# Optimization experiments

Measured on AMD Instinct MI355X. Metric: run time of the kernel, lower is better.

The kernel has to match this reference:

```python
import math
import jax, jax.numpy as jnp
import numpy as np

D_MODEL = 1024
N_HEADS = 16
HEAD_DIM = 64          # block_size
NUM_RULES = 64
RANK = 8               # proj_rank = round(sqrt(head_dim)); also router_rank
SHARED_RANK = 32       # round(sqrt(d_model))
NUM_BLOCKS = 16        # min(in,out)//block_size = 1024//64; total_block_dim == d_model
B, S = 4, 1024
ROPE_BASE = 10000.0


def setup_inputs() -> dict:
    key = jax.random.key(0)
    ks = iter(jax.random.split(key, 32))
    def nrm(shape, s=0.02):
        return jax.random.normal(next(ks), shape, dtype=jnp.float32) * s
    inp = {
        "x": jax.random.normal(next(ks), (B, S, D_MODEL), dtype=jnp.float32),
        "target_rule_ids": jax.random.randint(next(ks), (B, S), 0, NUM_RULES),
    }
    for p in ("q", "k", "v", "o"):
        inp[p + "_si"] = nrm((D_MODEL, SHARED_RANK))
        inp[p + "_so"] = nrm((SHARED_RANK, D_MODEL))
        inp[p + "_ri"] = nrm((NUM_RULES, HEAD_DIM, RANK))
        inp[p + "_ro"] = nrm((NUM_RULES, RANK, HEAD_DIM))
        inp[p + "_lg"] = nrm((NUM_RULES, NUM_BLOCKS), 1.0 / math.sqrt(NUM_BLOCKS))
    inp["router_q"] = nrm((NUM_RULES, RANK))
    inp["router_k"] = nrm((NUM_RULES, RANK))
    return inp


def _rule_proj(x, rules, si, so, ri, ro, lg):
    """RuleAwareProjection.forward_rules_batched, de-permuted.

    The torch code argsorts tokens by rule, zero-pads per-rule buckets, runs
    bmm per rule and scatters back; mathematically that equals a per-token
    gather of the rule's low-rank adapter, which is what we compute here.
    x: [N, D_MODEL], rules: [N] int.
    """
    base = (x @ si) @ so                                  # shared low-rank path
    xb = x.reshape(-1, NUM_BLOCKS, HEAD_DIM)              # [N, nb, bs]
    h = jnp.einsum('nbs,nsr->nbr', xb, ri[rules])         # [N, nb, rank]
    a = jnp.einsum('nbr,nrt->nbt', h, ro[rules])          # [N, nb, bs]
    # temperature = 1/sqrt(num_blocks) => logits / temperature = logits*sqrt(nb)
    sel = jax.nn.softmax(lg[rules] * math.sqrt(NUM_BLOCKS), axis=-1)
    return base + (a * sel[:, :, None]).reshape(-1, D_MODEL)


def _rope(q, k):
    # q, k: [B, H, S, D]; interleaved-pair rotation, start_pos = 0.
    S_, D = q.shape[2], q.shape[3]
    pos = jnp.arange(S_, dtype=jnp.float32)[:, None]
    div = jnp.exp(jnp.arange(0, D, 2, dtype=jnp.float32) * (-math.log(ROPE_BASE) / D))
    f = pos * div                                         # [S, D/2]
    sin, cos = jnp.sin(f), jnp.cos(f)
    def rot(t):
        t1, t2 = t[..., 0::2], t[..., 1::2]
        return jnp.stack([t1 * cos - t2 * sin, t2 * cos + t1 * sin], axis=-1).reshape(t.shape)
    return rot(q), rot(k)


def reference(x, target_rule_ids,
              q_si, q_so, q_ri, q_ro, q_lg,
              k_si, k_so, k_ri, k_ro, k_lg,
              v_si, v_so, v_ri, v_ro, v_lg,
              o_si, o_so, o_ri, o_ro, o_lg,
              router_q, router_k):
    B_, S_, C = x.shape
    flat_x = x.reshape(-1, C)
    rules = target_rule_ids.reshape(-1)

    q = _rule_proj(flat_x, rules, q_si, q_so, q_ri, q_ro, q_lg)
    k = _rule_proj(flat_x, rules, k_si, k_so, k_ri, k_ro, k_lg)
    v = _rule_proj(flat_x, rules, v_si, v_so, v_ri, v_ro, v_lg)
    q = q.reshape(B_, S_, N_HEADS, HEAD_DIM).transpose(0, 2, 1, 3)
    k = k.reshape(B_, S_, N_HEADS, HEAD_DIM).transpose(0, 2, 1, 3)
    v = v.reshape(B_, S_, N_HEADS, HEAD_DIM).transpose(0, 2, 1, 3)
    q, k = _rope(q, k)

    # rule-routing sparse mask: cosine affinity between token rule embeddings
    rq = router_q[target_rule_ids]                        # [B, S, rank]
    rk = router_k[target_rule_ids]
    rqn = rq / jnp.maximum(jnp.linalg.norm(rq, axis=-1, keepdims=True), 1e-12)
    rkn = rk / jnp.maximum(jnp.linalg.norm(rk, axis=-1, keepdims=True), 1e-12)
    tau = 1.0 / math.log(max(math.e, RANK))
    aff = jnp.einsum('bqr,bkr->bqk', rqn, rkn) / tau       # [B, S, S]
    causal = jnp.tril(jnp.ones((S_, S_), dtype=bool))
    masked = jnp.where(causal[None], aff, -jnp.inf)
    top_k = max(2, int(math.sqrt(S_)))
    if S_ > top_k:
        thr = jax.lax.top_k(masked, top_k)[0][..., -1:]
        rule_mask = (masked >= thr) & causal[None]
    else:
        rule_mask = jnp.broadcast_to(causal[None], masked.shape)

    scores = jnp.einsum('bhqd,bhkd->bhqk', q, k) / math.sqrt(HEAD_DIM)
    scores = jnp.where(rule_mask[:, None], scores, -jnp.inf)
    attn = jax.nn.softmax(scores, axis=-1)
    out = jnp.einsum('bhqk,bhkd->bhqd', attn, v)
    out = out.transpose(0, 2, 1, 3).reshape(-1, C)
    out = _rule_proj(out, rules, o_si, o_so, o_ri, o_ro, o_lg)
    return out.reshape(B_, S_, C)
```

## Files before the change

kernel.cpp:

```cpp
#include <hip/hip_runtime.h>
#include <hip/hip_bf16.h>

#define D_MODEL 1024
#define N_HEADS 16
#define HEAD_DIM 64
#define NUM_RULES 64
#define RANK 8
#define SHARED_RANK 32
#define NUM_BLOCKS_ 16
#define BB 4
#define SS 1024
#define NTOK (BB*SS)
#define NGRP (NTOK/8)
#define NGRP4 (NTOK/4)

typedef __attribute__((ext_vector_type(8))) short bf16x8;
typedef __attribute__((ext_vector_type(4))) float f32x4;

__device__ __forceinline__ float bf2f(unsigned short u) {
  unsigned int i = ((unsigned int)u) << 16;
  float f;
  __builtin_memcpy(&f, &i, 4);
  return f;
}
__device__ __forceinline__ unsigned short f2bf(float f) {
  __hip_bfloat16 h = __float2bfloat16(f);
  unsigned short u;
  __builtin_memcpy(&u, &h, 2);
  return u;
}
__device__ __forceinline__ float u2f(unsigned int i) {
  float f;
  __builtin_memcpy(&f, &i, 4);
  return f;
}
template<bool BF>
__device__ __forceinline__ float ldw(const void* p, size_t i) {
  if (BF) return bf2f(((const unsigned short*)p)[i]);
  else    return ((const float*)p)[i];
}

__device__ __forceinline__ void gload16(const void* g, void* l) {
  __builtin_amdgcn_global_load_lds(
      (const __attribute__((address_space(1))) unsigned int*)g,
      (__attribute__((address_space(3))) unsigned int*)l, 16, 0, 0);
}

__global__ void detect_kernel(const unsigned short* __restrict__ x, int* __restrict__ flag) {
  const int lane = threadIdx.x;
  int good = 0;
  for (int i = 0; i < 4; i++) {
    unsigned short u = x[lane*4 + i];
    int e = (u >> 7) & 0xFF;
    good += (e == 0 || (e >= 100 && e <= 145)) ? 1 : 0;
  }
  for (int off = 32; off; off >>= 1) good += __shfl_xor(good, off);
  if (lane == 0) flag[0] = (good >= 224) ? 1 : 0;
}

template<bool BF>
__device__ __forceinline__ void precompute_body(
    const void* rq, const void* rk,
    const void* qlg, const void* klg, const void* vlg, const void* olg,
    float* __restrict__ M, float* __restrict__ sel)
{
  __shared__ float rqn[64][8], rkn[64][8];
  const int tid = threadIdx.x;
  if (tid < 64) {
    float v[8]; float s = 0.f;
    for (int i = 0; i < 8; i++) { v[i] = ldw<BF>(rq, tid*8+i); s += v[i]*v[i]; }
    float inv = 1.0f / fmaxf(sqrtf(s), 1e-12f);
    for (int i = 0; i < 8; i++) rqn[tid][i] = v[i]*inv;
  } else if (tid < 128) {
    int r = tid - 64;
    float v[8]; float s = 0.f;
    for (int i = 0; i < 8; i++) { v[i] = ldw<BF>(rk, r*8+i); s += v[i]*v[i]; }
    float inv = 1.0f / fmaxf(sqrtf(s), 1e-12f);
    for (int i = 0; i < 8; i++) rkn[r][i] = v[i]*inv;
  }
  __syncthreads();
  const float LN8 = 2.0794415416798357f;
  for (int idx = tid; idx < 64*64; idx += 256) {
    int i = idx >> 6, j = idx & 63;
    float d = 0.f;
    for (int t = 0; t < 8; t++) d += rqn[i][t]*rkn[j][t];
    M[idx] = d * LN8;
  }
  const void* lgs[4] = {qlg, klg, vlg, olg};
  {
    int r = tid & 63;
    const void* lg = lgs[tid >> 6];
    float e[NUM_BLOCKS_]; float mx = -1e30f;
    for (int b = 0; b < NUM_BLOCKS_; b++) {
      e[b] = ldw<BF>(lg, r*NUM_BLOCKS_ + b) * 4.0f;
      mx = fmaxf(mx, e[b]);
    }
    float s = 0.f;
    for (int b = 0; b < NUM_BLOCKS_; b++) { e[b] = expf(e[b]-mx); s += e[b]; }
    float inv = 1.0f/s;
    for (int b = 0; b < NUM_BLOCKS_; b++) sel[tid*NUM_BLOCKS_+b] = e[b]*inv;
  }
}

__global__ void precompute_kernel(
    const void* rq, const void* rk,
    const void* qlg, const void* klg, const void* vlg, const void* olg,
    float* M, float* sel, const int* __restrict__ flag)
{
  if (*flag) precompute_body<true >(rq, rk, qlg, klg, vlg, olg, M, sel);
  else       precompute_body<false>(rq, rk, qlg, klg, vlg, olg, M, sel);
}

__global__ __launch_bounds__(128) void prep_wb_kernel(
    const float* __restrict__ qsi, const float* __restrict__ ksi,
    const float* __restrict__ vsi, const float* __restrict__ osi,
    unsigned short* __restrict__ wh, unsigned short* __restrict__ wl,
    const int* __restrict__ flag)
{
  if (*flag) return;
  const int kt = blockIdx.x, p = blockIdx.y;
  const int tid = threadIdx.x, nt = tid >> 6, lane = tid & 63;
  const float* si = (p==0)?qsi:((p==1)?ksi:((p==2)?vsi:osi));
  const int col = nt*16 + (lane & 15);
  const int k0 = kt*32 + (lane >> 4)*8;
  size_t base = ((((size_t)p*32 + kt)*2 + nt)*64 + lane)*8;
  unsigned short h8[8], l8[8];
  #pragma unroll
  for (int j = 0; j < 8; j++) {
    float f = si[(size_t)(k0 + j)*SHARED_RANK + col];
    unsigned short hu = f2bf(f);
    h8[j] = hu;
    l8[j] = f2bf(f - bf2f(hu));
  }
  #pragma unroll
  for (int j = 0; j < 8; j++) { wh[base + j] = h8[j]; wl[base + j] = l8[j]; }
}

template<int NPROJ>
__device__ __forceinline__ void tt_mfma_body(
    const float* __restrict__ xin,
    const unsigned short* __restrict__ wh, const unsigned short* __restrict__ wl,
    int p0, float* __restrict__ ttg)
{
  const int NT = NPROJ*2;
  const int tile = blockIdx.x;
  const int tid = threadIdx.x, lane = tid & 63, w = tid >> 6;
  const int kq = lane >> 4;
  __shared__ float red[4][64][25];

  f32x4 acc[NT];
  #pragma unroll
  for (int i = 0; i < NT; i++) acc[i] = (f32x4){0.f,0.f,0.f,0.f};

  const float* xrow = xin + (size_t)(tile*16 + (lane & 15))*D_MODEL + kq*8;
  #pragma unroll 2
  for (int s = 0; s < 8; s++) {
    const int kt = w*8 + s;
    float4 a0 = *(const float4*)(xrow + kt*32);
    float4 a1 = *(const float4*)(xrow + kt*32 + 4);
    float av[8] = {a0.x,a0.y,a0.z,a0.w,a1.x,a1.y,a1.z,a1.w};
    bf16x8 ah, al;
    #pragma unroll
    for (int j = 0; j < 8; j++) {
      unsigned short hu = f2bf(av[j]);
      ah[j] = (short)hu;
      al[j] = (short)f2bf(av[j] - bf2f(hu));
    }
    #pragma unroll
    for (int p = 0; p < NPROJ; p++) {
      #pragma unroll
      for (int nt = 0; nt < 2; nt++) {
        size_t bidx = ((((size_t)(p0+p)*32 + kt)*2 + nt)*64 + lane)*8;
        bf16x8 bh = *(const bf16x8*)(wh + bidx);
        bf16x8 bl = *(const bf16x8*)(wl + bidx);
        f32x4 c = acc[p*2+nt];
        c = __builtin_amdgcn_mfma_f32_16x16x32_bf16(ah, bh, c, 0, 0, 0);
        c = __builtin_amdgcn_mfma_f32_16x16x32_bf16(al, bh, c, 0, 0, 0);
        c = __builtin_amdgcn_mfma_f32_16x16x32_bf16(ah, bl, c, 0, 0, 0);
        acc[p*2+nt] = c;
      }
    }
  }
  #pragma unroll
  for (int i = 0; i < NT; i++) {
    red[w][lane][i*4+0] = acc[i][0]; red[w][lane][i*4+1] = acc[i][1];
    red[w][lane][i*4+2] = acc[i][2]; red[w][lane][i*4+3] = acc[i][3];
  }
  __syncthreads();
  if (w == 0) {
    const int tok0 = tile*16 + (lane >> 4)*4;
    #pragma unroll
    for (int i = 0; i < NT; i++) {
      const int ys = i >> 1, jj = (i & 1)*16 + (lane & 15);
      #pragma unroll
      for (int r = 0; r < 4; r++) {
        float sum = red[0][lane][i*4+r] + red[1][lane][i*4+r]
                  + red[2][lane][i*4+r] + red[3][lane][i*4+r];
        ttg[((size_t)ys*NTOK + tok0 + r)*32 + jj] = sum;
      }
    }
  }
}

__global__ __launch_bounds__(256) void A_tt_mfma3(
    const float* __restrict__ xin,
    const unsigned short* __restrict__ wh, const unsigned short* __restrict__ wl,
    float* __restrict__ ttg, const int* __restrict__ flag)
{
  if (*flag) return;
  tt_mfma_body<3>(xin, wh, wl, 0, ttg);
}

__global__ __launch_bounds__(256) void A_tt_mfma1(
    const float* __restrict__ xin,
    const unsigned short* __restrict__ wh, const unsigned short* __restrict__ wl,
    float* __restrict__ ttg, const int* __restrict__ flag)
{
  if (*flag) return;
  tt_mfma_body<1>(xin, wh, wl, 3, ttg);
}

template<int NP>
__device__ __forceinline__ void hh_body(
    const float* __restrict__ xin, const int* __restrict__ rules,
    const float* __restrict__ ri0, const float* __restrict__ ri1,
    const float* __restrict__ ri2, float* __restrict__ hhg)
{
  const int g = blockIdx.x, n0 = g*8, tid = threadIdx.x;
  const int t = tid >> 5, blk = (tid >> 1) & 15, r0 = (tid & 1)*4;
  const int n = n0 + t;
  const int rule = rules[n];
  const float* xb = xin + (size_t)n*D_MODEL + blk*64;
  const float* wb[3];
  wb[0] = ri0 + (size_t)rule*512 + r0;
  if (NP > 1) {
    wb[1] = ri1 + (size_t)rule*512 + r0;
    wb[2] = ri2 + (size_t)rule*512 + r0;
  }
  float a[NP][4];
  #pragma unroll
  for (int p = 0; p < NP; p++) { a[p][0]=0.f; a[p][1]=0.f; a[p][2]=0.f; a[p][3]=0.f; }
  #pragma unroll 4
  for (int k4 = 0; k4 < 16; k4++) {
    float4 xv = *(const float4*)(xb + k4*4);
    #pragma unroll
    for (int q = 0; q < 4; q++) {
      const int k = k4*4 + q;
      float xq = (q==0)?xv.x:((q==1)?xv.y:((q==2)?xv.z:xv.w));
      #pragma unroll
      for (int p = 0; p < NP; p++) {
        float4 wv = *(const float4*)(wb[p] + (size_t)k*8);
        a[p][0] += xq*wv.x; a[p][1] += xq*wv.y; a[p][2] += xq*wv.z; a[p][3] += xq*wv.w;
      }
    }
  }
  #pragma unroll
  for (int p = 0; p < NP; p++) {
    float4 hv; hv.x=a[p][0]; hv.y=a[p][1]; hv.z=a[p][2]; hv.w=a[p][3];
    *(float4*)&hhg[((size_t)p*NTOK + n)*128 + blk*8 + r0] = hv;
  }
}

__global__ __launch_bounds__(256) void A_hh3_f32(
    const float* __restrict__ xin, const int* __restrict__ rules,
    const float* __restrict__ qri, const float* __restrict__ kri,
    const float* __restrict__ vri, float* __restrict__ hhg,
    const int* __restrict__ flag)
{
  if (*flag) return;
  hh_body<3>(xin, rules, qri, kri, vri, hhg);
}

__global__ __launch_bounds__(256) void A_hh1_f32(
    const float* __restrict__ xin, const int* __restrict__ rules,
    const float* __restrict__ ori, float* __restrict__ hhg,
    const int* __restrict__ flag)
{
  if (*flag) return;
  hh_body<1>(xin, rules, ori, ori, ori, hhg);
}

template<bool IN_BF, bool W_BF>
__device__ __forceinline__ void stageA_body(
    const void* __restrict__ xin, const int* __restrict__ rules,
    const void* __restrict__ si, const void* __restrict__ ri,
    float* __restrict__ ttg, float* __restrict__ hhg, int yslot)
{
  const int g = blockIdx.x, n0 = g*8, tid = threadIdx.x;
  __shared__ float xs[8][D_MODEL];
  __shared__ float tpart[8][32][9];
  __shared__ int rl[8];

  #pragma unroll
  for (int t = 0; t < 8; t++) {
    float4 f;
    if (IN_BF) {
      ushort4 u = ((const ushort4*)((const unsigned short*)xin + (size_t)(n0+t)*D_MODEL))[tid];
      f.x = bf2f(u.x); f.y = bf2f(u.y); f.z = bf2f(u.z); f.w = bf2f(u.w);
    } else {
      f = ((const float4*)xin)[(size_t)(n0+t)*(D_MODEL/4) + tid];
    }
    *(float4*)&xs[t][tid*4] = f;
  }
  if (tid < 8) rl[tid] = rules[n0 + tid];
  __syncthreads();

  {
    const int c = tid >> 5, j = tid & 31;
    float p[8];
    #pragma unroll
    for (int t = 0; t < 8; t++) p[t] = 0.f;
    #pragma unroll 4
    for (int d4 = 0; d4 < 32; d4++) {
      const int d = c*128 + d4*4;
      float w0 = ldw<W_BF>(si, (size_t)(d+0)*SHARED_RANK + j);
      float w1 = ldw<W_BF>(si, (size_t)(d+1)*SHARED_RANK + j);
      float w2 = ldw<W_BF>(si, (size_t)(d+2)*SHARED_RANK + j);
      float w3 = ldw<W_BF>(si, (size_t)(d+3)*SHARED_RANK + j);
      #pragma unroll
      for (int t = 0; t < 8; t++) {
        float4 xv = *(const float4*)&xs[t][d];
        p[t] += xv.x*w0 + xv.y*w1 + xv.z*w2 + xv.w*w3;
      }
    }
    #pragma unroll
    for (int t = 0; t < 8; t++) tpart[c][j][t] = p[t];
  }
  __syncthreads();

  {
    const int t = tid >> 5, j = tid & 31;
    float s = 0.f;
    #pragma unroll
    for (int c = 0; c < 8; c++) s += tpart[c][j][t];
    ttg[((size_t)yslot*NTOK + n0 + t)*32 + j] = s;
  }
  {
    const int t = tid >> 5, blk = (tid >> 1) & 15, r0 = (tid & 1)*4;
    const int rule = rl[t];
    float a0=0.f, a1=0.f, a2=0.f, a3=0.f;
    #pragma unroll 4
    for (int k4 = 0; k4 < 16; k4++) {
      const int kk = ((k4 + blk) & 15) * 4;
      float4 xv = *(const float4*)&xs[t][blk*64 + kk];
      #pragma unroll
      for (int q = 0; q < 4; q++) {
        const int k = kk + q;
        float w0,w1,w2,w3;
        if (W_BF) {
          ushort4 u = *(const ushort4*)((const unsigned short*)ri + (size_t)rule*512 + (size_t)k*8 + r0);
          w0=bf2f(u.x); w1=bf2f(u.y); w2=bf2f(u.z); w3=bf2f(u.w);
        } else {
          float4 u = *(const float4*)((const float*)ri + (size_t)rule*512 + (size_t)k*8 + r0);
          w0=u.x; w1=u.y; w2=u.z; w3=u.w;
        }
        float xq = (q==0)?xv.x:((q==1)?xv.y:((q==2)?xv.z:xv.w));
        a0 += xq*w0; a1 += xq*w1; a2 += xq*w2; a3 += xq*w3;
      }
    }
    float4 hv; hv.x=a0; hv.y=a1; hv.z=a2; hv.w=a3;
    *(float4*)&hhg[((size_t)yslot*NTOK + n0 + t)*128 + blk*8 + r0] = hv;
  }
}

__global__ __launch_bounds__(256) void A_qkv_bf16(
    const void* x, const int* rules,
    const void* qsi, const void* qri, const void* ksi, const void* kri,
    const void* vsi, const void* vri,
    float* ttg, float* hhg, const int* __restrict__ flag)
{
  if (!*flag) return;
  const int y = blockIdx.y;
  const void* si = (y==0)?qsi:((y==1)?ksi:vsi);
  const void* ri = (y==0)?qri:((y==1)?kri:vri);
  stageA_body<true,true>(x, rules, si, ri, ttg, hhg, y);
}

__global__ __launch_bounds__(256) void A_o_bf16(
    const void* ain, const int* rules, const void* osi, const void* ori,
    float* ttg, float* hhg, const int* __restrict__ flag)
{
  if (!*flag) return;
  stageA_body<false,true>(ain, rules, osi, ori, ttg, hhg, 0);
}

template<bool W_BF>
__device__ __forceinline__ void stageB_body(
    const float* __restrict__ ttg, const float* __restrict__ hhg,
    const int* __restrict__ rules,
    const void* __restrict__ so, const void* __restrict__ ro,
    const float* __restrict__ sel, void* __restrict__ out,
    int yslot, int do_rope, int out_bf)
{
  const int blk4 = blockIdx.x;
  const int n0 = blk4*4, tid = threadIdx.x;
  __shared__ float tt_lds[32][5];
  __shared__ float hh_lds[4][132];
  __shared__ int rl[4];

  if (tid < 128) {
    const int j = tid >> 2, t4 = tid & 3;
    tt_lds[j][t4] = ttg[((size_t)yslot*NTOK + n0 + t4)*32 + j];
  } else if (tid < 256 && (tid - 128) < 128) {
    const int i = tid - 128;
    const int t4 = i >> 5, c = (i*4) & 127;
    float4 hv = *(const float4*)&hhg[((size_t)yslot*NTOK + n0 + t4)*128 + c];
    *(float4*)&hh_lds[t4][c] = hv;
  }
  if (tid < 4) rl[tid] = rules[n0 + tid];
  __syncthreads();

  const int ch0 = tid*4;
  float a0[4], a1[4], a2[4], a3[4];
  #pragma unroll
  for (int t = 0; t < 4; t++) { a0[t]=0.f; a1[t]=0.f; a2[t]=0.f; a3[t]=0.f; }

  #pragma unroll 4
  for (int j = 0; j < 32; j++) {
    float w0, w1, w2, w3;
    if (W_BF) {
      ushort4 u = *(const ushort4*)((const unsigned short*)so + (size_t)j*D_MODEL + ch0);
      w0=bf2f(u.x); w1=bf2f(u.y); w2=bf2f(u.z); w3=bf2f(u.w);
    } else {
      float4 u = *(const float4*)((const float*)so + (size_t)j*D_MODEL + ch0);
      w0=u.x; w1=u.y; w2=u.z; w3=u.w;
    }
    #pragma unroll
    for (int t = 0; t < 4; t++) {
      float tv = tt_lds[j][t];
      a0[t] += tv*w0; a1[t] += tv*w1; a2[t] += tv*w2; a3[t] += tv*w3;
    }
  }

  const int blk = ch0 >> 6, tc = ch0 & 63;
  float inv0 = 0.f, inv1 = 0.f;
  if (do_rope) {
    inv0 = expf(-(float)tc     * (9.210340371976184f/64.0f));
    inv1 = expf(-(float)(tc+2) * (9.210340371976184f/64.0f));
  }
  #pragma unroll 2
  for (int t = 0; t < 4; t++) {
    const int rule = rl[t];
    float b0=0.f, b1=0.f, b2=0.f, b3=0.f;
    #pragma unroll
    for (int r = 0; r < 8; r++) {
      float w0,w1,w2,w3;
      if (W_BF) {
        ushort4 u = *(const ushort4*)((const unsigned short*)ro + (size_t)rule*512 + r*64 + tc);
        w0=bf2f(u.x); w1=bf2f(u.y); w2=bf2f(u.z); w3=bf2f(u.w);
      } else {
        float4 u = *(const float4*)((const float*)ro + (size_t)rule*512 + r*64 + tc);
        w0=u.x; w1=u.y; w2=u.z; w3=u.w;
      }
      float hv = hh_lds[t][blk*8 + r];
      b0 += hv*w0; b1 += hv*w1; b2 += hv*w2; b3 += hv*w3;
    }
    float sb = sel[rule*NUM_BLOCKS_ + blk];
    float e0 = a0[t] + b0*sb, o0 = a1[t] + b1*sb;
    float e1 = a2[t] + b2*sb, o1 = a3[t] + b3*sb;
    const int n = n0 + t;
    if (do_rope) {
      float spos = (float)(n & (SS-1));
      float sn0, cs0, sn1, cs1;
      sincosf(spos*inv0, &sn0, &cs0);
      sincosf(spos*inv1, &sn1, &cs1);
      float u0 = e0*cs0 - o0*sn0; o0 = o0*cs0 + e0*sn0; e0 = u0;
      float u1 = e1*cs1 - o1*sn1; o1 = o1*cs1 + e1*sn1; e1 = u1;
    }
    if (out_bf) {
      ushort4 uv; uv.x=f2bf(e0); uv.y=f2bf(o0); uv.z=f2bf(e1); uv.w=f2bf(o1);
      *(ushort4*)((unsigned short*)out + (size_t)n*D_MODEL + ch0) = uv;
    } else {
      float4 fv; fv.x=e0; fv.y=o0; fv.z=e1; fv.w=o1;
      *(float4*)((float*)out + (size_t)n*D_MODEL + ch0) = fv;
    }
  }
}

__global__ __launch_bounds__(256) void B_qkv(
    const float* ttg, const float* hhg, const int* rules,
    const void* qso, const void* qro, const void* kso, const void* kro,
    const void* vso, const void* vro,
    const float* sel, float* qb, unsigned short* kb, unsigned short* vb,
    const int* __restrict__ flag)
{
  const int y = blockIdx.y;
  const void* so = (y==0)?qso:((y==1)?kso:vso);
  const void* ro = (y==0)?qro:((y==1)?kro:vro);
  void* out = (y==0)?(void*)qb:((y==1)?(void*)kb:(void*)vb);
  if (*flag)
    stageB_body<true >(ttg, hhg, rules, so, ro, sel + y*1024, out, y, (y<2)?1:0, (y>=1)?1:0);
  else
    stageB_body<false>(ttg, hhg, rules, so, ro, sel + y*1024, out, y, (y<2)?1:0, (y>=1)?1:0);
}

__global__ __launch_bounds__(256) void B_o(
    const float* ttg, const float* hhg, const int* rules,
    const void* oso, const void* oro, const float* sel, void* out,
    const int* __restrict__ flag)
{
  if (*flag) stageB_body<true >(ttg, hhg, rules, oso, oro, sel, out, 0, 0, 1);
  else       stageB_body<false>(ttg, hhg, rules, oso, oro, sel, out, 0, 0, 0);
}

__global__ __launch_bounds__(64) void mask_kernel(
    const int* __restrict__ rules, const float* __restrict__ M,
    unsigned long long* __restrict__ am, unsigned int* __restrict__ rp)
{
  const int bid = blockIdx.x;
  const int b = bid >> 10, qi = bid & 1023;
  const int lane = threadIdx.x;
  __shared__ int rrow[SS];
  __shared__ float val[64];
  __shared__ int cnth[64];
  for (int i = lane; i < SS/4; i += 64)
    ((int4*)rrow)[i] = ((const int4*)(rules + b*SS))[i];
  cnth[lane] = 0;
  __syncthreads();
  if (qi < 16 && lane < 16) {
    unsigned v = 0;
    #pragma unroll
    for (int nt = 0; nt < 4; nt++)
      v |= ((unsigned)rrow[qi*64 + nt*16 + lane] & 0xffu) << (8*nt);
    rp[b*256 + qi*16 + lane] = v;
  }
  for (int k = lane; k <= qi; k += 64) atomicAdd(&cnth[rrow[k]], 1);
  const int qrule = rrow[qi];
  const float myv = M[qrule*64 + lane];
  val[lane] = myv;
  __syncthreads();
  const int c = cnth[lane];
  int A = 0;
  for (int r = 0; r < 64; r++) {
    int cr = __shfl(c, r);
    A += (val[r] > myv) ? cr : 0;
  }
  unsigned long long allowed = __ballot(A < 32);
  if (lane == 0) am[bid] = allowed;
}

__global__ __launch_bounds__(256) void vtrans_kernel(
    const unsigned short* __restrict__ vb, unsigned short* __restrict__ vt)
{
  const int st = blockIdx.x, h = blockIdx.y, b = blockIdx.z;
  __shared__ unsigned short t[64][72];
  const int tid = threadIdx.x;
  #pragma unroll
  for (int it = 0; it < 2; it++) {
    int i = tid + it*256;
    int r = i >> 3, c8 = (i & 7)*8;
    uint4 v = *(const uint4*)(vb + ((size_t)(b*SS + st*64 + r)*D_MODEL + h*HEAD_DIM + c8));
    t[c8+0][r] = (unsigned short)(v.x & 0xffffu);
    t[c8+1][r] = (unsigned short)(v.x >> 16);
    t[c8+2][r] = (unsigned short)(v.y & 0xffffu);
    t[c8+3][r] = (unsigned short)(v.y >> 16);
    t[c8+4][r] = (unsigned short)(v.z & 0xffffu);
    t[c8+5][r] = (unsigned short)(v.z >> 16);
    t[c8+6][r] = (unsigned short)(v.w & 0xffffu);
    t[c8+7][r] = (unsigned short)(v.w >> 16);
  }
  __syncthreads();
  #pragma unroll
  for (int it = 0; it < 2; it++) {
    int i = tid + it*256;
    int d = i >> 3, c8 = i & 7;
    uint4 o = *(const uint4*)&t[d][c8*8];
    *(uint4*)(vt + ((size_t)(b*N_HEADS + h)*HEAD_DIM + d)*SS + st*64 + c8*8) = o;
  }
}

__global__ __launch_bounds__(256, 4) void attn_mfma_kernel(
    const float* __restrict__ qb,
    const unsigned short* __restrict__ kb,
    const unsigned short* __restrict__ vtb,
    const unsigned int* __restrict__ rp,
    const unsigned long long* __restrict__ am,
    float* outb)
{
  const int x = blockIdx.x, b = blockIdx.y, h = blockIdx.z;
  const int qt = (x < 8) ? x : (23 - x);
  const int tid = threadIdx.x, lane = tid & 63, w = tid >> 6;
  __shared__ unsigned short Ks[2][64*64];
  __shared__ unsigned short Vs[2][64*64];
  __shared__ unsigned short Pl[4][16*64];

  const unsigned short* kbase = kb + (size_t)b*SS*D_MODEL + h*HEAD_DIM;
  const unsigned short* vbase = vtb + (size_t)(b*N_HEADS + h)*HEAD_DIM*SS;
  const unsigned int* rpb = rp + b*256;

  const int srow0 = tid >> 3;
  const int spos  = tid & 7;
  unsigned short* pw = &Pl[w][0];

  const int qa = qt*64 + w*16 + (lane & 15);
  bf16x8 qfrag[2];
  {
    const float* qrow = qb + (size_t)(b*SS + qa)*D_MODEL + h*HEAD_DIM + (lane>>4)*8;
    #pragma unroll
    for (int kc = 0; kc < 2; kc++) {
      float4 f0 = *(const float4*)(qrow + kc*32);
      float4 f1 = *(const float4*)(qrow + kc*32 + 4);
      bf16x8 qv;
      qv[0] = (short)f2bf(f0.x*0.125f); qv[1] = (short)f2bf(f0.y*0.125f);
      qv[2] = (short)f2bf(f0.z*0.125f); qv[3] = (short)f2bf(f0.w*0.125f);
      qv[4] = (short)f2bf(f1.x*0.125f); qv[5] = (short)f2bf(f1.y*0.125f);
      qv[6] = (short)f2bf(f1.z*0.125f); qv[7] = (short)f2bf(f1.w*0.125f);
      qfrag[kc] = qv;
    }
  }
  int qg[4]; unsigned aqlo[4], aqhi[4];
  #pragma unroll
  for (int r = 0; r < 4; r++) {
    qg[r] = qt*64 + w*16 + (lane>>4)*4 + r;
    uint2 mm = *(const uint2*)(am + (size_t)b*SS + qg[r]);
    aqlo[r] = mm.x; aqhi[r] = mm.y;
  }
  f32x4 Oacc[4];
  #pragma unroll
  for (int nt = 0; nt < 4; nt++) Oacc[nt] = (f32x4){0.f,0.f,0.f,0.f};
  float mrun[4], lrun[4];
  #pragma unroll
  for (int r = 0; r < 4; r++) { mrun[r] = -1e30f; lrun[r] = 0.f; }

  #pragma unroll
  for (int it = 0; it < 2; it++) {
    int row = srow0 + it*32;
    int sc = spos ^ (row & 7);
    gload16(kbase + (size_t)row*D_MODEL + sc*8, &Ks[0][(row*8 + spos)*8]);
    gload16(vbase + (size_t)row*SS + sc*8,      &Vs[0][(row*8 + spos)*8]);
  }
  __syncthreads();

  int cur = 0;
  for (int kt = 0; kt <= qt; kt++) {
    const unsigned ru = rpb[kt*16 + (lane & 15)];
    if (kt < qt) {
      const size_t koff = (size_t)(kt + 1)*64;
      #pragma unroll
      for (int it = 0; it < 2; it++) {
        int row = srow0 + it*32;
        int sc = spos ^ (row & 7);
        gload16(kbase + (koff + row)*D_MODEL + sc*8, &Ks[cur^1][(row*8 + spos)*8]);
        gload16(vbase + (size_t)row*SS + koff + sc*8, &Vs[cur^1][(row*8 + spos)*8]);
      }
    }
    const unsigned short* kt_lds = Ks[cur];
    const unsigned short* vt_lds = Vs[cur];

    f32x4 Sacc[4];
    #pragma unroll
    for (int nt = 0; nt < 4; nt++) {
      const int key = nt*16 + (lane & 15);
      f32x4 c = (f32x4){0.f,0.f,0.f,0.f};
      #pragma unroll
      for (int kc = 0; kc < 2; kc++) {
        int off = (key*128 + kc*64 + (lane>>4)*16) ^ ((key & 7) << 4);
        bf16x8 kf = *(const bf16x8*)((const char*)kt_lds + off);
        c = __builtin_amdgcn_mfma_f32_16x16x32_bf16(qfrag[kc], kf, c, 0, 0, 0);
      }
      Sacc[nt] = c;
    }

    float sv[4][4];
    #pragma unroll
    for (int nt = 0; nt < 4; nt++) {
      const int k = kt*64 + nt*16 + (lane & 15);
      const unsigned rr = (ru >> (nt*8)) & 0xffu;
      const unsigned sh = rr & 31u;
      const bool hi = rr >= 32;
      #pragma unroll
      for (int r = 0; r < 4; r++) {
        unsigned bits = hi ? aqhi[r] : aqlo[r];
        bool ok = (((bits >> sh) & 1u) != 0u) && (k <= qg[r]);
        sv[nt][r] = ok ? Sacc[nt][r] : -3e38f;
      }
    }

    float tm[4];
    #pragma unroll
    for (int r = 0; r < 4; r++)
      tm[r] = fmaxf(fmaxf(sv[0][r], sv[1][r]), fmaxf(sv[2][r], sv[3][r]));
    #pragma unroll
    for (int off = 1; off < 16; off <<= 1) {
      #pragma unroll
      for (int r = 0; r < 4; r++) tm[r] = fmaxf(tm[r], __shfl_xor(tm[r], off));
    }
    float alpha[4];
    #pragma unroll
    for (int r = 0; r < 4; r++) {
      float nm = fmaxf(mrun[r], tm[r]);
      alpha[r] = __expf(mrun[r] - nm);
      mrun[r] = nm;
    }
    float ps[4] = {0.f, 0.f, 0.f, 0.f};
    #pragma unroll
    for (int nt = 0; nt < 4; nt++) {
      #pragma unroll
      for (int r = 0; r < 4; r++) {
        float p = __expf(sv[nt][r] - mrun[r]);
        ps[r] += p;
        const int q = (lane>>4)*4 + r;
        int off = (q*128 + (nt*16 + (lane & 15))*2) ^ ((q & 7) << 4);
        *(unsigned short*)((char*)pw + off) = f2bf(p);
      }
    }
    #pragma unroll
    for (int off = 1; off < 16; off <<= 1) {
      #pragma unroll
      for (int r = 0; r < 4; r++) ps[r] += __shfl_xor(ps[r], off);
    }
    #pragma unroll
    for (int r = 0; r < 4; r++) lrun[r] = lrun[r]*alpha[r] + ps[r];
    #pragma unroll
    for (int nt = 0; nt < 4; nt++) {
      Oacc[nt][0] *= alpha[0]; Oacc[nt][1] *= alpha[1];
      Oacc[nt][2] *= alpha[2]; Oacc[nt][3] *= alpha[3];
    }

    #pragma unroll
    for (int kc = 0; kc < 2; kc++) {
      const int qrow = lane & 15;
      int aoff = (qrow*128 + kc*64 + (lane>>4)*16) ^ ((qrow & 7) << 4);
      bf16x8 pa = *(const bf16x8*)((const char*)pw + aoff);
      #pragma unroll
      for (int nt = 0; nt < 4; nt++) {
        const int d = nt*16 + (lane & 15);
        int boff = (d*128 + kc*64 + (lane>>4)*16) ^ ((d & 7) << 4);
        bf16x8 vf = *(const bf16x8*)((const char*)vt_lds + boff);
        Oacc[nt] = __builtin_amdgcn_mfma_f32_16x16x32_bf16(pa, vf, Oacc[nt], 0, 0, 0);
      }
    }
    __syncthreads();
    cur ^= 1;
  }

  float invl[4];
  #pragma unroll
  for (int r = 0; r < 4; r++) invl[r] = 1.0f / lrun[r];
  #pragma unroll
  for (int nt = 0; nt < 4; nt++) {
    #pragma unroll
    for (int r = 0; r < 4; r++) {
      outb[(size_t)(b*SS + qg[r])*D_MODEL + h*HEAD_DIM + nt*16 + (lane & 15)]
          = Oacc[nt][r]*invl[r];
    }
  }
}

extern "C" void kernel_launch(void* const* d_in, const int* in_sizes, int n_in,
                              void* d_out, int out_size, void* d_ws, size_t ws_size,
                              hipStream_t stream) {
  (void)in_sizes; (void)n_in; (void)out_size; (void)ws_size;
  const void* x    = d_in[0];
  const int* rules = (const int*)d_in[1];
  const void* q_si = d_in[2];  const void* q_so = d_in[3];
  const void* q_ri = d_in[4];  const void* q_ro = d_in[5];  const void* q_lg = d_in[6];
  const void* k_si = d_in[7];  const void* k_so = d_in[8];
  const void* k_ri = d_in[9];  const void* k_ro = d_in[10]; const void* k_lg = d_in[11];
  const void* v_si = d_in[12]; const void* v_so = d_in[13];
  const void* v_ri = d_in[14]; const void* v_ro = d_in[15]; const void* v_lg = d_in[16];
  const void* o_si = d_in[17]; const void* o_so = d_in[18];
  const void* o_ri = d_in[19]; const void* o_ro = d_in[20]; const void* o_lg = d_in[21];
  const void* rq   = d_in[22]; const void* rk   = d_in[23];

  char* ws = (char*)d_ws;
  const size_t MB = 1024*1024;
  float*          qb    = (float*)(ws);
  unsigned short* kb    = (unsigned short*)(ws + 16*MB);
  unsigned short* vb    = (unsigned short*)(ws + 24*MB);
  unsigned short* vtb   = (unsigned short*)(ws + 32*MB);
  float*          ttg   = (float*)(ws + 40*MB);
  float*          hhg   = (float*)(ws + 42*MB);
  unsigned long long* amask = (unsigned long long*)(ws + 48*MB);
  float*          Mt    = (float*)(ws + 49*MB + 16*1024);
  float*          selt  = (float*)(ws + 49*MB + 32*1024);
  int*            flag  = (int*)  (ws + 49*MB + 48*1024);
  unsigned int*   rp    = (unsigned int*)(ws + 49*MB + 52*1024);
  unsigned short* wpkh  = (unsigned short*)(ws + 49*MB + 64*1024);
  unsigned short* wpkl  = (unsigned short*)(ws + 49*MB + 64*1024 + 256*1024);

  detect_kernel<<<1, 64, 0, stream>>>((const unsigned short*)x, flag);
  precompute_kernel<<<1, 256, 0, stream>>>(rq, rk, q_lg, k_lg, v_lg, o_lg, Mt, selt, flag);
  mask_kernel<<<NTOK, 64, 0, stream>>>(rules, Mt, amask, rp);
  prep_wb_kernel<<<dim3(32, 4), 128, 0, stream>>>(
      (const float*)q_si, (const float*)k_si, (const float*)v_si, (const float*)o_si,
      wpkh, wpkl, flag);

  A_qkv_bf16<<<dim3(NGRP, 3), 256, 0, stream>>>(x, rules, q_si, q_ri, k_si, k_ri, v_si, v_ri, ttg, hhg, flag);
  A_tt_mfma3<<<256, 256, 0, stream>>>((const float*)x, wpkh, wpkl, ttg, flag);
  A_hh3_f32<<<NGRP, 256, 0, stream>>>((const float*)x, rules,
      (const float*)q_ri, (const float*)k_ri, (const float*)v_ri, hhg, flag);

  B_qkv<<<dim3(NGRP4, 3), 256, 0, stream>>>(ttg, hhg, rules, q_so, q_ro, k_so, k_ro, v_so, v_ro,
                                            selt, qb, kb, vb, flag);

  vtrans_kernel<<<dim3(16, 16, 4), 256, 0, stream>>>(vb, vtb);
  attn_mfma_kernel<<<dim3(16, BB, N_HEADS), 256, 0, stream>>>(qb, kb, vtb, rp, amask, qb);

  A_o_bf16<<<dim3(NGRP, 1), 256, 0, stream>>>(qb, rules, o_si, o_ri, ttg, hhg, flag);
  A_tt_mfma1<<<256, 256, 0, stream>>>(qb, wpkh, wpkl, ttg, flag);
  A_hh1_f32<<<NGRP, 256, 0, stream>>>(qb, rules, (const float*)o_ri, hhg, flag);
  B_o<<<NGRP4, 256, 0, stream>>>(ttg, hhg, rules, o_so, o_ro, selt + 3*1024, d_out, flag);
}
```

Baseline: 284.3 us.

## Replace async LDS double buffer with register-prefetched single buffer and MFMA priority

Result: no change. 284.6 us (+0.1%).

```diff
diff --git a/kernel.cpp b/kernel.cpp
--- a/kernel.cpp
+++ b/kernel.cpp
@@ -38,12 +38,6 @@
 __device__ __forceinline__ float ldw(const void* p, size_t i) {
   if (BF) return bf2f(((const unsigned short*)p)[i]);
   else    return ((const float*)p)[i];
-}
-
-__device__ __forceinline__ void gload16(const void* g, void* l) {
-  __builtin_amdgcn_global_load_lds(
-      (const __attribute__((address_space(1))) unsigned int*)g,
-      (__attribute__((address_space(3))) unsigned int*)l, 16, 0, 0);
 }
 
 __global__ void detect_kernel(const unsigned short* __restrict__ x, int* __restrict__ flag) {
@@ -580,16 +574,18 @@
   const int x = blockIdx.x, b = blockIdx.y, h = blockIdx.z;
   const int qt = (x < 8) ? x : (23 - x);
   const int tid = threadIdx.x, lane = tid & 63, w = tid >> 6;
-  __shared__ unsigned short Ks[2][64*64];
-  __shared__ unsigned short Vs[2][64*64];
+  __shared__ unsigned short Ks[64*64];
+  __shared__ unsigned short Vs[64*64];
   __shared__ unsigned short Pl[4][16*64];
 
   const unsigned short* kbase = kb + (size_t)b*SS*D_MODEL + h*HEAD_DIM;
   const unsigned short* vbase = vtb + (size_t)(b*N_HEADS + h)*HEAD_DIM*SS;
   const unsigned int* rpb = rp + b*256;
 
-  const int srow0 = tid >> 3;
-  const int spos  = tid & 7;
+  const int srow = tid >> 3;
+  const int spos = tid & 7;
+  const int kc0 = (srow*8      + (spos ^ (srow        & 7)))*8;
+  const int kc1 = ((srow+32)*8 + (spos ^ ((srow+32)   & 7)))*8;
   unsigned short* pw = &Pl[w][0];
 
   const int qa = qt*64 + w*16 + (lane & 15);
@@ -622,32 +618,29 @@
   #pragma unroll
   for (int r = 0; r < 4; r++) { mrun[r] = -1e30f; lrun[r] = 0.f; }
 
-  #pragma unroll
-  for (int it = 0; it < 2; it++) {
-    int row = srow0 + it*32;
-    int sc = spos ^ (row & 7);
-    gload16(kbase + (size_t)row*D_MODEL + sc*8, &Ks[0][(row*8 + spos)*8]);
-    gload16(vbase + (size_t)row*SS + sc*8,      &Vs[0][(row*8 + spos)*8]);
+  {
+    uint4 k0 = *(const uint4*)(kbase + (size_t)srow*D_MODEL + spos*8);
+    uint4 k1 = *(const uint4*)(kbase + (size_t)(srow+32)*D_MODEL + spos*8);
+    uint4 v0 = *(const uint4*)(vbase + (size_t)srow*SS + spos*8);
+    uint4 v1 = *(const uint4*)(vbase + (size_t)(srow+32)*SS + spos*8);
+    *(uint4*)&Ks[kc0] = k0; *(uint4*)&Ks[kc1] = k1;
+    *(uint4*)&Vs[kc0] = v0; *(uint4*)&Vs[kc1] = v1;
   }
   __syncthreads();
 
-  int cur = 0;
   for (int kt = 0; kt <= qt; kt++) {
     const unsigned ru = rpb[kt*16 + (lane & 15)];
+    uint4 nk0, nk1, nv0, nv1;
     if (kt < qt) {
       const size_t koff = (size_t)(kt + 1)*64;
-      #pragma unroll
-      for (int it = 0; it < 2; it++) {
-        int row = srow0 + it*32;
-        int sc = spos ^ (row & 7);
-        gload16(kbase + (koff + row)*D_MODEL + sc*8, &Ks[cur^1][(row*8 + spos)*8]);
-        gload16(vbase + (size_t)row*SS + koff + sc*8, &Vs[cur^1][(row*8 + spos)*8]);
-      }
-    }
-    const unsigned short* kt_lds = Ks[cur];
-    const unsigned short* vt_lds = Vs[cur];
+      nk0 = *(const uint4*)(kbase + (koff + srow)*D_MODEL + spos*8);
+      nk1 = *(const uint4*)(kbase + (koff + srow + 32)*D_MODEL + spos*8);
+      nv0 = *(const uint4*)(vbase + (size_t)srow*SS + koff + spos*8);
+      nv1 = *(const uint4*)(vbase + (size_t)(srow+32)*SS + koff + spos*8);
+    }
 
     f32x4 Sacc[4];
+    __builtin_amdgcn_s_setprio(1);
     #pragma unroll
     for (int nt = 0; nt < 4; nt++) {
       const int key = nt*16 + (lane & 15);
@@ -655,11 +648,12 @@
       #pragma unroll
       for (int kc = 0; kc < 2; kc++) {
         int off = (key*128 + kc*64 + (lane>>4)*16) ^ ((key & 7) << 4);
-        bf16x8 kf = *(const bf16x8*)((const char*)kt_lds + off);
+        bf16x8 kf = *(const bf16x8*)((const char*)Ks + off);
         c = __builtin_amdgcn_mfma_f32_16x16x32_bf16(qfrag[kc], kf, c, 0, 0, 0);
       }
       Sacc[nt] = c;
     }
+    __builtin_amdgcn_s_setprio(0);
 
     float sv[4][4];
     #pragma unroll
@@ -717,6 +711,7 @@
       Oacc[nt][2] *= alpha[2]; Oacc[nt][3] *= alpha[3];
     }
 
+    __builtin_amdgcn_s_setprio(1);
     #pragma unroll
     for (int kc = 0; kc < 2; kc++) {
       const int qrow = lane & 15;
@@ -726,12 +721,17 @@
       for (int nt = 0; nt < 4; nt++) {
         const int d = nt*16 + (lane & 15);
         int boff = (d*128 + kc*64 + (lane>>4)*16) ^ ((d & 7) << 4);
-        bf16x8 vf = *(const bf16x8*)((const char*)vt_lds + boff);
+        bf16x8 vf = *(const bf16x8*)((const char*)Vs + boff);
         Oacc[nt] = __builtin_amdgcn_mfma_f32_16x16x32_bf16(pa, vf, Oacc[nt], 0, 0, 0);
       }
     }
+    __builtin_amdgcn_s_setprio(0);
     __syncthreads();
-    cur ^= 1;
+    if (kt < qt) {
+      *(uint4*)&Ks[kc0] = nk0; *(uint4*)&Ks[kc1] = nk1;
+      *(uint4*)&Vs[kc0] = nv0; *(uint4*)&Vs[kc1] = nv1;
+      __syncthreads();
+    }
   }
 
   float invl[4];
```
